# Kernel optimization log

Measured on AMD Instinct MI355X. Metric: run time of the kernel, lower is better.

Reference implementation:

```python
import jax, jax.numpy as jnp
import numpy as np

N, E, F, B = 4096, 8192, 256, 16


def setup_inputs() -> dict:
    key = jax.random.key(0)
    k_x, k_idx, k_w, k_b = jax.random.split(key, 4)
    x = jax.random.normal(k_x, (B, E, F), dtype=jnp.float32)
    # Incidence matrix: each edge (column) connects 2 random distinct nodes.
    ends = jax.random.randint(k_idx, (2, E), 0, N)  # [2, E] node ids per edge
    cols = jnp.arange(E)
    inci = jnp.zeros((N, E), dtype=jnp.float32)
    inci = inci.at[ends[0], cols].set(1.0).at[ends[1], cols].set(1.0)
    w = jax.random.normal(k_w, (N, E), dtype=jnp.float32) * 0.05
    b = jax.random.normal(k_b, (N, E), dtype=jnp.float32) * 0.01
    return {"x": x, "inci": inci, "w": w, "b": b}


def reference(x, inci, w, b):
    # (w * inci + b) @ x : [N,E] x [B,E,F] -> [B,N,F]
    m = w * inci + b
    return jnp.einsum("ne,bef->bnf", m, x)
```

## Files before the change

### kernel.cpp

```cpp
#include <hip/hip_runtime.h>
#include <hip/hip_bf16.h>

#define Ndim 4096
#define Edim 8192
#define Fdim 256
#define Bdim 16
#define EB (Edim * 2)
#define NT (Edim / 64)

typedef __attribute__((ext_vector_type(8))) short bf16x8;
typedef __attribute__((ext_vector_type(4))) float f32x4;

__device__ __forceinline__ unsigned short f2bf(float f) {
  unsigned int u = __float_as_uint(f);
  u += 0x7fffu + ((u >> 16) & 1u);
  return (unsigned short)(u >> 16);
}

__device__ __forceinline__ void gload_lds16(const void* g, void* l) {
  __builtin_amdgcn_global_load_lds(
      (const __attribute__((address_space(1))) unsigned int*)g,
      (__attribute__((address_space(3))) unsigned int*)l, 16, 0, 0);
}

__device__ __forceinline__ void stage_half(const char* g, char* d) {
  gload_lds16(g, d);
  gload_lds16(g + (size_t)64 * EB, d + 8192);
}

#define RD(base, r, kk) \
  (*(const bf16x8*)((base) + (r) * 128 + ((((kk) * 64) + khi) ^ (((r) & 7) << 4))))

__global__ void convert_m(const float* __restrict__ w, const float* __restrict__ inc,
                          const float* __restrict__ bb, unsigned short* __restrict__ m) {
  size_t i = ((size_t)blockIdx.x * 256 + threadIdx.x) * 4;
  float4 wv = *(const float4*)(w + i);
  float4 iv = *(const float4*)(inc + i);
  float4 bv = *(const float4*)(bb + i);
  ushort4 o;
  o.x = f2bf(fmaf(wv.x, iv.x, bv.x));
  o.y = f2bf(fmaf(wv.y, iv.y, bv.y));
  o.z = f2bf(fmaf(wv.z, iv.z, bv.z));
  o.w = f2bf(fmaf(wv.w, iv.w, bv.w));
  *(ushort4*)(m + i) = o;
}

__global__ void transpose_x(const float* __restrict__ x, unsigned short* __restrict__ xT) {
  __shared__ unsigned short tile[64][66];
  int e0 = blockIdx.x * 64, f0 = blockIdx.y * 64, b = blockIdx.z;
  const float* xb = x + (size_t)b * Edim * Fdim;
  unsigned short* xTb = xT + (size_t)b * Fdim * Edim;
  int t = threadIdx.x;
  int fl = t & 63, rq = t >> 6;
#pragma unroll
  for (int i = 0; i < 16; i++) {
    int el = rq * 16 + i;
    float v = xb[(size_t)(e0 + el) * Fdim + f0 + fl];
    tile[el][fl] = f2bf(v);
  }
  __syncthreads();
  int ep = (t & 31) * 2;
  int fr0 = t >> 5;
#pragma unroll
  for (int j = 0; j < 8; j++) {
    int fr = fr0 + j * 8;
    unsigned int pk = (unsigned int)tile[ep][fr] | ((unsigned int)tile[ep + 1][fr] << 16);
    *(unsigned int*)&xTb[(size_t)(f0 + fr) * Edim + e0 + ep] = pk;
  }
}

template <int MODE>
__device__ __forceinline__ void ktile(
    const char* lA, const char* lB, const char* lAn, const char* lBn,
    char* d1, const char* g1, char* d2, const char* g2,
    char* d3, const char* g3, char* d4, const char* g4,
    int lane, int wr, int wc,
    bf16x8 (&aCur)[8], bf16x8 (&bLoC)[4], f32x4 acc[8][4]) {
  const int l15 = lane & 15;
  const int khi = (lane >> 4) << 4;
  bf16x8 bHi[4], aHi[8];

  if constexpr (MODE >= 1) stage_half(g1, d1);
  __builtin_amdgcn_s_barrier();
  __builtin_amdgcn_s_setprio(1);
#pragma unroll
  for (int m = 0; m < 4; ++m)
#pragma unroll
    for (int n = 0; n < 2; ++n)
#pragma unroll
      for (int kk = 0; kk < 2; ++kk)
        acc[m][n] = __builtin_amdgcn_mfma_f32_16x16x32_bf16(aCur[m * 2 + kk], bLoC[n * 2 + kk],
                                                            acc[m][n], 0, 0, 0);
  __builtin_amdgcn_s_setprio(0);
#pragma unroll
  for (int n = 0; n < 2; ++n)
#pragma unroll
    for (int kk = 0; kk < 2; ++kk)
      bHi[n * 2 + kk] = RD(lB, wc * 64 + (n + 2) * 16 + l15, kk);
  __builtin_amdgcn_s_barrier();

  if constexpr (MODE >= 1) stage_half(g2, d2);
  __builtin_amdgcn_s_barrier();
  __builtin_amdgcn_s_setprio(1);
#pragma unroll
  for (int m = 0; m < 4; ++m)
#pragma unroll
    for (int n = 0; n < 2; ++n)
#pragma unroll
      for (int kk = 0; kk < 2; ++kk)
        acc[m][n + 2] = __builtin_amdgcn_mfma_f32_16x16x32_bf16(aCur[m * 2 + kk], bHi[n * 2 + kk],
                                                                acc[m][n + 2], 0, 0, 0);
  __builtin_amdgcn_s_setprio(0);
#pragma unroll
  for (int m = 0; m < 4; ++m)
#pragma unroll
    for (int kk = 0; kk < 2; ++kk)
      aHi[m * 2 + kk] = RD(lA, wr * 128 + 64 + m * 16 + l15, kk);
  __builtin_amdgcn_s_barrier();

  if constexpr (MODE == 2) stage_half(g3, d3);
  __builtin_amdgcn_s_barrier();
  __builtin_amdgcn_s_setprio(1);
#pragma unroll
  for (int m = 0; m < 4; ++m)
#pragma unroll
    for (int n = 0; n < 2; ++n)
#pragma unroll
      for (int kk = 0; kk < 2; ++kk)
        acc[m + 4][n] = __builtin_amdgcn_mfma_f32_16x16x32_bf16(aHi[m * 2 + kk], bLoC[n * 2 + kk],
                                                                acc[m + 4][n], 0, 0, 0);
  __builtin_amdgcn_s_setprio(0);
  if constexpr (MODE == 2) asm volatile("s_waitcnt vmcnt(2)" ::: "memory");
  if constexpr (MODE == 1) asm volatile("s_waitcnt vmcnt(0)" ::: "memory");
  if constexpr (MODE >= 1) {
#pragma unroll
    for (int n = 0; n < 2; ++n)
#pragma unroll
      for (int kk = 0; kk < 2; ++kk)
        bLoC[n * 2 + kk] = RD(lBn, wc * 64 + n * 16 + l15, kk);
  }
  __builtin_amdgcn_s_barrier();

  if constexpr (MODE == 2) stage_half(g4, d4);
  __builtin_amdgcn_s_barrier();
  __builtin_amdgcn_s_setprio(1);
#pragma unroll
  for (int m = 0; m < 4; ++m)
#pragma unroll
    for (int n = 0; n < 2; ++n)
#pragma unroll
      for (int kk = 0; kk < 2; ++kk)
        acc[m + 4][n + 2] = __builtin_amdgcn_mfma_f32_16x16x32_bf16(aHi[m * 2 + kk], bHi[n * 2 + kk],
                                                                    acc[m + 4][n + 2], 0, 0, 0);
  __builtin_amdgcn_s_setprio(0);
  if constexpr (MODE >= 1) {
#pragma unroll
    for (int m = 0; m < 4; ++m)
#pragma unroll
      for (int kk = 0; kk < 2; ++kk)
        aCur[m * 2 + kk] = RD(lAn, wr * 128 + m * 16 + l15, kk);
  }
  __builtin_amdgcn_s_barrier();
}

__global__ __launch_bounds__(512, 2) void gemm8(
    const unsigned short* __restrict__ A,
    const unsigned short* __restrict__ Bt,
    float* __restrict__ C) {
  __shared__ __align__(16) char smem[131072];

  const int bid = blockIdx.x;
  const int lid = ((bid & 7) << 5) | (bid >> 3);
  const int mt = lid >> 4;
  const int bb = lid & 15;

  const int tid = threadIdx.x;
  const int lane = tid & 63;
  const int w = tid >> 6;
  const int wr = w >> 2;
  const int wc = w & 3;
  const int l15 = lane & 15;
  const int khi = (lane >> 4) << 4;

  const int r0 = tid >> 3;
  const int c0 = ((tid & 7) ^ (r0 & 7)) << 4;

  const char* Ag = (const char*)A + (size_t)(mt * 256) * EB + (size_t)r0 * EB + c0;
  const char* Bg = (const char*)Bt + (size_t)(bb * 256) * EB + (size_t)r0 * EB + c0;
  char* dst = smem + tid * 16;

  f32x4 acc[8][4];
#pragma unroll
  for (int m = 0; m < 8; ++m)
#pragma unroll
    for (int n = 0; n < 4; ++n) acc[m][n] = (f32x4){0.f, 0.f, 0.f, 0.f};

  const size_t HEB = (size_t)128 * EB;

  stage_half(Ag, dst);
  stage_half(Ag + HEB, dst + 16384);
  stage_half(Bg, dst + 32768);
  stage_half(Bg + HEB, dst + 49152);
  stage_half(Bg + 128, dst + 98304);
  stage_half(Bg + 128 + HEB, dst + 114688);
  asm volatile("s_waitcnt vmcnt(4)" ::: "memory");
  __builtin_amdgcn_s_barrier();

  bf16x8 aCur[8];
  bf16x8 bLoC[4];
#pragma unroll
  for (int m = 0; m < 4; ++m)
#pragma unroll
    for (int kk = 0; kk < 2; ++kk)
      aCur[m * 2 + kk] = RD((const char*)smem, wr * 128 + m * 16 + l15, kk);
#pragma unroll
  for (int n = 0; n < 2; ++n)
#pragma unroll
    for (int kk = 0; kk < 2; ++kk)
      bLoC[n * 2 + kk] = RD((const char*)smem + 32768, wc * 64 + n * 16 + l15, kk);

  for (int i = 0; i < NT / 2 - 1; ++i) {
    const size_t t1b = (size_t)(2 * i + 1) * 128;
    const size_t t2b = (size_t)(2 * i + 2) * 128;
    const size_t t3b = (size_t)(2 * i + 3) * 128;
    ktile<2>(smem, smem + 32768, smem + 65536, smem + 98304,
             dst + 65536, Ag + t1b,
             dst + 81920, Ag + t1b + HEB,
             dst + 32768, Bg + t2b,
             dst + 49152, Bg + t2b + HEB,
             lane, wr, wc, aCur, bLoC, acc);
    ktile<2>(smem + 65536, smem + 98304, smem, smem + 32768,
             dst, Ag + t2b,
             dst + 16384, Ag + t2b + HEB,
             dst + 98304, Bg + t3b,
             dst + 114688, Bg + t3b + HEB,
             lane, wr, wc, aCur, bLoC, acc);
  }
  {
    const size_t tlb = (size_t)(NT - 1) * 128;
    ktile<1>(smem, smem + 32768, smem + 65536, smem + 98304,
             dst + 65536, Ag + tlb,
             dst + 81920, Ag + tlb + HEB,
             nullptr, nullptr, nullptr, nullptr,
             lane, wr, wc, aCur, bLoC, acc);
    ktile<0>(smem + 65536, smem + 98304, nullptr, nullptr,
             nullptr, nullptr, nullptr, nullptr,
             nullptr, nullptr, nullptr, nullptr,
             lane, wr, wc, aCur, bLoC, acc);
  }

  float* Cb = C + (size_t)bb * (Ndim * Fdim) + (size_t)(mt * 256) * Fdim;
#pragma unroll
  for (int m = 0; m < 8; ++m) {
    int row0 = wr * 128 + m * 16 + ((lane >> 4) << 2);
#pragma unroll
    for (int n = 0; n < 4; ++n) {
      int col = wc * 64 + n * 16 + (lane & 15);
#pragma unroll
      for (int j = 0; j < 4; ++j)
        Cb[(size_t)(row0 + j) * Fdim + col] = acc[m][n][j];
    }
  }
}

__global__ void naive_kernel(const float* __restrict__ x, const float* __restrict__ inci,
                             const float* __restrict__ w, const float* __restrict__ b,
                             float* __restrict__ out) {
  int n = blockIdx.x & (Ndim - 1);
  int bb = blockIdx.x >> 12;
  int f = threadIdx.x;
  const float* xb = x + (size_t)bb * Edim * Fdim;
  const size_t nE = (size_t)n * Edim;
  float acc = 0.f;
  for (int e = 0; e < Edim; e++) {
    float m = fmaf(w[nE + e], inci[nE + e], b[nE + e]);
    acc = fmaf(m, xb[(size_t)e * Fdim + f], acc);
  }
  out[(size_t)bb * Ndim * Fdim + (size_t)n * Fdim + f] = acc;
}

extern "C" void kernel_launch(void* const* d_in, const int* in_sizes, int n_in,
                              void* d_out, int out_size, void* d_ws, size_t ws_size,
                              hipStream_t stream) {
  const float* x = (const float*)d_in[0];
  const float* inci = (const float*)d_in[1];
  const float* w = (const float*)d_in[2];
  const float* b = (const float*)d_in[3];
  float* out = (float*)d_out;

  size_t mBytes = (size_t)Ndim * Edim * 2;
  size_t xTBytes = (size_t)Bdim * Fdim * Edim * 2;
  if (ws_size >= mBytes + xTBytes) {
    unsigned short* m_bf = (unsigned short*)d_ws;
    unsigned short* xT = m_bf + (size_t)Ndim * Edim;
    convert_m<<<(Ndim * (size_t)Edim) / 4 / 256, 256, 0, stream>>>(w, inci, b, m_bf);
    transpose_x<<<dim3(Edim / 64, Fdim / 64, Bdim), 256, 0, stream>>>(x, xT);
    gemm8<<<256, 512, 0, stream>>>(m_bf, xT, out);
  } else {
    naive_kernel<<<Bdim * Ndim, 256, 0, stream>>>(x, inci, w, b, out);
  }
}
```

Baseline: 331.6 us.

## Restructure GEMM pipeline to issue full next-tile prefetch once per k-tile with two barriers

Replaces the per-quarter staging, where each quarter of the MFMA work was bracketed by two barriers and one prefetch slice, with a schedule that runs three MFMA quarters without barriers. It then waits on outstanding loads, syncs once, and issues all four global-to-LDS loads for tile t+2 before the last quarter. The prologue now preloads two full tiles, and the loop is a simple double-buffered loop over every k-tile. This cuts barrier count per tile from eight to two to reduce synchronization stalls. In exchange, the waits on loads are coarser (vmcnt(0)), which can expose more memory latency.

```diff
diff --git a/kernel.cpp b/kernel.cpp
--- a/kernel.cpp
+++ b/kernel.cpp
@@ -30,6 +30,8 @@
 
 #define RD(base, r, kk) \
   (*(const bf16x8*)((base) + (r) * 128 + ((((kk) * 64) + khi) ^ (((r) & 7) << 4))))
+
+#define FENCE() asm volatile("" ::: "memory")
 
 __global__ void convert_m(const float* __restrict__ w, const float* __restrict__ inc,
                           const float* __restrict__ bb, unsigned short* __restrict__ m) {
@@ -80,8 +82,6 @@
   const int khi = (lane >> 4) << 4;
   bf16x8 bHi[4], aHi[8];
 
-  if constexpr (MODE >= 1) stage_half(g1, d1);
-  __builtin_amdgcn_s_barrier();
   __builtin_amdgcn_s_setprio(1);
 #pragma unroll
   for (int m = 0; m < 4; ++m)
@@ -97,10 +97,7 @@
 #pragma unroll
     for (int kk = 0; kk < 2; ++kk)
       bHi[n * 2 + kk] = RD(lB, wc * 64 + (n + 2) * 16 + l15, kk);
-  __builtin_amdgcn_s_barrier();
-
-  if constexpr (MODE >= 1) stage_half(g2, d2);
-  __builtin_amdgcn_s_barrier();
+
   __builtin_amdgcn_s_setprio(1);
 #pragma unroll
   for (int m = 0; m < 4; ++m)
@@ -116,10 +113,7 @@
 #pragma unroll
     for (int kk = 0; kk < 2; ++kk)
       aHi[m * 2 + kk] = RD(lA, wr * 128 + 64 + m * 16 + l15, kk);
-  __builtin_amdgcn_s_barrier();
-
-  if constexpr (MODE == 2) stage_half(g3, d3);
-  __builtin_amdgcn_s_barrier();
+
   __builtin_amdgcn_s_setprio(1);
 #pragma unroll
   for (int m = 0; m < 4; ++m)
@@ -130,19 +124,23 @@
         acc[m + 4][n] = __builtin_amdgcn_mfma_f32_16x16x32_bf16(aHi[m * 2 + kk], bLoC[n * 2 + kk],
                                                                 acc[m + 4][n], 0, 0, 0);
   __builtin_amdgcn_s_setprio(0);
-  if constexpr (MODE == 2) asm volatile("s_waitcnt vmcnt(2)" ::: "memory");
-  if constexpr (MODE == 1) asm volatile("s_waitcnt vmcnt(0)" ::: "memory");
   if constexpr (MODE >= 1) {
+    asm volatile("s_waitcnt vmcnt(0)" ::: "memory");
+    __builtin_amdgcn_s_barrier();
+    FENCE();
 #pragma unroll
     for (int n = 0; n < 2; ++n)
 #pragma unroll
       for (int kk = 0; kk < 2; ++kk)
         bLoC[n * 2 + kk] = RD(lBn, wc * 64 + n * 16 + l15, kk);
   }
-  __builtin_amdgcn_s_barrier();
-
-  if constexpr (MODE == 2) stage_half(g4, d4);
-  __builtin_amdgcn_s_barrier();
+
+  if constexpr (MODE == 2) {
+    stage_half(g1, d1);
+    stage_half(g2, d2);
+    stage_half(g3, d3);
+    stage_half(g4, d4);
+  }
   __builtin_amdgcn_s_setprio(1);
 #pragma unroll
   for (int m = 0; m < 4; ++m)
@@ -159,8 +157,9 @@
 #pragma unroll
       for (int kk = 0; kk < 2; ++kk)
         aCur[m * 2 + kk] = RD(lAn, wr * 128 + m * 16 + l15, kk);
-  }
-  __builtin_amdgcn_s_barrier();
+    __builtin_amdgcn_s_barrier();
+    FENCE();
+  }
 }
 
 __global__ __launch_bounds__(512, 2) void gemm8(
@@ -201,10 +200,13 @@
   stage_half(Ag + HEB, dst + 16384);
   stage_half(Bg, dst + 32768);
   stage_half(Bg + HEB, dst + 49152);
+  stage_half(Ag + 128, dst + 65536);
+  stage_half(Ag + 128 + HEB, dst + 81920);
   stage_half(Bg + 128, dst + 98304);
   stage_half(Bg + 128 + HEB, dst + 114688);
-  asm volatile("s_waitcnt vmcnt(4)" ::: "memory");
+  asm volatile("s_waitcnt vmcnt(8)" ::: "memory");
   __builtin_amdgcn_s_barrier();
+  FENCE();
 
   bf16x8 aCur[8];
   bf16x8 bLoC[4];
@@ -219,35 +221,29 @@
     for (int kk = 0; kk < 2; ++kk)
       bLoC[n * 2 + kk] = RD((const char*)smem + 32768, wc * 64 + n * 16 + l15, kk);
 
-  for (int i = 0; i < NT / 2 - 1; ++i) {
-    const size_t t1b = (size_t)(2 * i + 1) * 128;
-    const size_t t2b = (size_t)(2 * i + 2) * 128;
-    const size_t t3b = (size_t)(2 * i + 3) * 128;
-    ktile<2>(smem, smem + 32768, smem + 65536, smem + 98304,
-             dst + 65536, Ag + t1b,
-             dst + 81920, Ag + t1b + HEB,
-             dst + 32768, Bg + t2b,
-             dst + 49152, Bg + t2b + HEB,
+  for (int t = 0; t < NT - 2; ++t) {
+    const int u = t & 1;
+    const char* lA = smem + u * 65536;
+    const char* lB = lA + 32768;
+    const char* lAn = smem + (u ^ 1) * 65536;
+    const char* lBn = lAn + 32768;
+    char* du = dst + u * 65536;
+    const size_t kb = (size_t)(t + 2) * 128;
+    ktile<2>(lA, lB, lAn, lBn,
+             du, Ag + kb,
+             du + 16384, Ag + kb + HEB,
+             du + 32768, Bg + kb,
+             du + 49152, Bg + kb + HEB,
              lane, wr, wc, aCur, bLoC, acc);
-    ktile<2>(smem + 65536, smem + 98304, smem, smem + 32768,
-             dst, Ag + t2b,
-             dst + 16384, Ag + t2b + HEB,
-             dst + 98304, Bg + t3b,
-             dst + 114688, Bg + t3b + HEB,
-             lane, wr, wc, aCur, bLoC, acc);
-  }
-  {
-    const size_t tlb = (size_t)(NT - 1) * 128;
-    ktile<1>(smem, smem + 32768, smem + 65536, smem + 98304,
-             dst + 65536, Ag + tlb,
-             dst + 81920, Ag + tlb + HEB,
-             nullptr, nullptr, nullptr, nullptr,
-             lane, wr, wc, aCur, bLoC, acc);
-    ktile<0>(smem + 65536, smem + 98304, nullptr, nullptr,
-             nullptr, nullptr, nullptr, nullptr,
-             nullptr, nullptr, nullptr, nullptr,
-             lane, wr, wc, aCur, bLoC, acc);
-  }
+  }
+  ktile<1>(smem, smem + 32768, smem + 65536, smem + 98304,
+           nullptr, nullptr, nullptr, nullptr,
+           nullptr, nullptr, nullptr, nullptr,
+           lane, wr, wc, aCur, bLoC, acc);
+  ktile<0>(smem + 65536, smem + 98304, nullptr, nullptr,
+           nullptr, nullptr, nullptr, nullptr,
+           nullptr, nullptr, nullptr, nullptr,
+           lane, wr, wc, aCur, bLoC, acc);
 
   float* Cb = C + (size_t)bb * (Ndim * Fdim) + (size_t)(mt * 256) * Fdim;
 #pragma unroll
```

Measured after the change: 363.0 us. 1.09x slower.
